# Kernel tuning notes

Hardware: AMD Instinct MI355X
Metric: run time of the kernel (lower is better)

The kernel has to match this reference:

```python
import jax, jax.numpy as jnp
import numpy as np

E = 256        # HP.EMBED_SIZE
R = 8          # number of derivation rules / MLPs
S = 512        # number of sequential derivation steps
N = 256        # nodes produced per step
N_INIT = 1024  # initial axiom (thax) embeddings
TOTAL = N_INIT + S * N  # 132096 rows in the vectors buffer
M = 65536      # masked nodes fed to eval_net


def setup_inputs() -> dict:
    key = jax.random.key(0)
    ks = jax.random.split(key, 12)
    rng = np.random.default_rng(0)

    init_vecs = jax.random.normal(ks[0], (N_INIT, E), jnp.float32)
    # rule MLPs: concat(2 parents) -> E (relu) -> E
    W1 = jax.random.normal(ks[1], (R, 2 * E, E), jnp.float32) * (1.0 / np.sqrt(2 * E))
    b1 = jnp.zeros((R, E), jnp.float32)
    W2 = jax.random.normal(ks[2], (R, E, E), jnp.float32) * (1.0 / np.sqrt(E))
    b2 = jnp.zeros((R, E), jnp.float32)
    # eval net: E -> E (relu) -> 1
    eval_W1 = jax.random.normal(ks[3], (E, E), jnp.float32) * (1.0 / np.sqrt(E))
    eval_b1 = jnp.zeros((E,), jnp.float32)
    eval_W2 = jax.random.normal(ks[4], (E, 1), jnp.float32) * (1.0 / np.sqrt(E))
    eval_b2 = jnp.zeros((1,), jnp.float32)

    # step s writes rows [N_INIT + s*N, N_INIT + (s+1)*N)
    ind_steps = (N_INIT + np.arange(S * N, dtype=np.int32)).reshape(S, N)
    # parents drawn causally from already-computed prefix [0, N_INIT + s*N)
    highs = (N_INIT + np.arange(S, dtype=np.int64) * N)[:, None, None]
    pars_ind_steps = (rng.random((S, N, 2)) * highs).astype(np.int32)
    rule_steps = rng.integers(0, R, size=(S,)).astype(np.int32)
    mask = rng.integers(0, TOTAL, size=(M,)).astype(np.int32)

    pos = jax.random.uniform(ks[5], (M,), jnp.float32)
    neg = jax.random.uniform(ks[6], (M,), jnp.float32)
    target = jnp.round(jax.random.uniform(ks[7], (M,), jnp.float32))

    return {
        'init_vecs': init_vecs, 'W1': W1, 'b1': b1, 'W2': W2, 'b2': b2,
        'eval_W1': eval_W1, 'eval_b1': eval_b1, 'eval_W2': eval_W2, 'eval_b2': eval_b2,
        'pos': pos, 'neg': neg, 'target': target,
        'ind_steps': jnp.asarray(ind_steps), 'pars_ind_steps': jnp.asarray(pars_ind_steps),
        'rule_steps': jnp.asarray(rule_steps), 'mask': jnp.asarray(mask),
    }


def reference(init_vecs, W1, b1, W2, b2, eval_W1, eval_b1, eval_W2, eval_b2,
              pos, neg, target, ind_steps, pars_ind_steps, rule_steps, mask):
    vectors = jnp.zeros((TOTAL, E), init_vecs.dtype).at[:N_INIT].set(init_vecs)

    def step(vec, xs):
        inds, pars, r = xs            # [N], [N,2], scalar rule id
        p = vec[pars].reshape(N, 2 * E)   # gather parents
        h = jax.nn.relu(p @ W1[r] + b1[r])
        out = h @ W2[r] + b2[r]
        return vec.at[inds].set(out), None  # scatter new node embeddings

    vectors, _ = jax.lax.scan(step, vectors, (ind_steps, pars_ind_steps, rule_steps))

    x = vectors[mask]
    val = (jax.nn.relu(x @ eval_W1 + eval_b1) @ eval_W2 + eval_b2)[:, 0]

    # pos_weight = POS_WEIGHT_EXTRA * tot_neg / tot_pos (constant w.r.t. grads)
    pw = jax.lax.stop_gradient(jnp.sum(neg) / jnp.maximum(jnp.sum(pos), 1.0))
    # BCEWithLogitsLoss(pos_weight, reduction='none')
    contrib = pw * target * jax.nn.softplus(-val) + (1.0 - target) * jax.nn.softplus(val)
    loss = jnp.sum((pos + neg) * contrib)
    posOK = jnp.sum(pos * (val >= 0))
    negOK = jnp.sum(neg * (val < 0))
    return loss, posOK, negOK
```

## Files before the change

kernel.cpp:

```cpp
#include <hip/hip_runtime.h>
#include <math.h>

#define EMB   256
#define TWOE  512
#define NINIT 1024
#define NSTEP 512
#define NPS   256
#define TOTAL (NINIT + NSTEP * NPS)
#define MM    65536
#define NNODE (NSTEP * NPS)
#define NKEY  2048
#define BTH   512
#define TROWS 32
#define CHK_SH  16384
#define RULE_SH (24 * CHK_SH)

typedef short s16x8 __attribute__((ext_vector_type(8)));
typedef float f32x4 __attribute__((ext_vector_type(4)));

#define OFF_VECH   0ull
#define OFF_VECL   ((size_t)TOTAL * EMB * 2)
#define OFF_VAL    (2ull * (size_t)TOTAL * EMB * 2)
#define OFF_CNT    (OFF_VAL + (size_t)MM * 4)
#define OFF_ACC    (OFF_CNT + 4096)
#define OFF_PW     (OFF_ACC + 64)
#define OFF_KCNT   (OFF_PW + 192)
#define OFF_KOFS   (OFF_KCNT + (size_t)NKEY * 4)
#define OFF_NL     (OFF_KOFS + (size_t)NKEY * 4)
#define OFF_BROWS  (OFF_NL + 256)
#define OFF_LVL8   (OFF_BROWS + (size_t)NNODE * 4)
#define OFF_WSPLIT (OFF_LVL8 + 132352)


__device__ __forceinline__ void store_dev_u32(unsigned* p, unsigned v) {
  asm volatile("global_store_dword %0, %1, off sc0 sc1" :: "v"(p), "v"(v) : "memory");
}
__device__ __forceinline__ void store_dev_b64(void* p, uint2 v) {
  asm volatile("global_store_dwordx2 %0, %1, off sc0 sc1" :: "v"(p), "v"(v) : "memory");
}
__device__ __forceinline__ void store_dev_b128(void* p, uint4 v) {
  store_dev_b64(p, make_uint2(v.x, v.y));
  store_dev_b64((char*)p + 8, make_uint2(v.z, v.w));
}
__device__ __forceinline__ unsigned load_dev_u32(const unsigned* p) {
  unsigned r;
  asm volatile("global_load_dword %0, %1, off sc0 sc1\n\ts_waitcnt vmcnt(0)"
               : "=v"(r) : "v"(p) : "memory");
  return r;
}

__device__ __forceinline__ void gbar_full(unsigned* gc, unsigned* gep) {
  asm volatile("s_waitcnt vmcnt(0)" ::: "memory");
  __syncthreads();
  if (threadIdx.x == 0) {
    unsigned old = __hip_atomic_fetch_add(gc, 1u, __ATOMIC_RELAXED, __HIP_MEMORY_SCOPE_AGENT);
    unsigned tgt = old / 256u + 1u;
    if ((old & 255u) == 255u) store_dev_u32(gep, tgt);
    else while (load_dev_u32(gep) < tgt) __builtin_amdgcn_s_sleep(1);
  }
  __syncthreads();
}

__device__ __forceinline__ void split8(const float* f, uint4& h4, uint4& l4) {
  unsigned hu[8], lu[8];
  #pragma unroll
  for (int i = 0; i < 8; ++i) {
    unsigned u = __builtin_bit_cast(unsigned, f[i]);
    float rh = __builtin_bit_cast(float, u & 0xffff0000u);
    float rl = f[i] - rh;
    hu[i] = u >> 16;
    lu[i] = __builtin_bit_cast(unsigned, rl) >> 16;
  }
  h4 = make_uint4(hu[0] | (hu[1] << 16), hu[2] | (hu[3] << 16),
                  hu[4] | (hu[5] << 16), hu[6] | (hu[7] << 16));
  l4 = make_uint4(lu[0] | (lu[1] << 16), lu[2] | (lu[3] << 16),
                  lu[4] | (lu[5] << 16), lu[6] | (lu[7] << 16));
}

__global__ void zero_scratch(unsigned* cnt, double* acc) {
  for (int i = threadIdx.x; i < 1024; i += 256) cnt[i] = 0u;
  if (threadIdx.x < 8) acc[threadIdx.x] = 0.0;
}

__global__ void init_convert(const float* __restrict__ src,
                             unsigned short* __restrict__ vh,
                             unsigned short* __restrict__ vl) {
  int slot = blockIdx.x * blockDim.x + threadIdx.x;
  float f[8];
  *(float4*)&f[0] = reinterpret_cast<const float4*>(src)[slot * 2];
  *(float4*)&f[4] = reinterpret_cast<const float4*>(src)[slot * 2 + 1];
  uint4 h4, l4;
  split8(f, h4, l4);
  *(uint4*)(vh + (size_t)slot * 8) = h4;
  *(uint4*)(vl + (size_t)slot * 8) = l4;
}

__global__ __launch_bounds__(512)
void presplit(const float* __restrict__ W1, const float* __restrict__ W2,
              short* __restrict__ Ws)
{
  const int blk = blockIdx.x;
  const int r = blk / 24, c = blk % 24;
  const float* src; int kbase;
  if (c < 16) { src = W1 + (size_t)r * TWOE * EMB; kbase = c * 32; }
  else        { src = W2 + (size_t)r * EMB * EMB;  kbase = (c - 16) * 32; }
  short* dst = Ws + (size_t)blk * CHK_SH;
  const int tid = threadIdx.x;
  #pragma unroll
  for (int u = 0; u < 2; ++u) {
    int qq = tid + u * 512;
    int g = qq >> 6, l = qq & 63;
    const float* p = src + (size_t)(kbase + ((l >> 4) << 3)) * EMB + (g << 4) + (l & 15);
    float f[8];
    #pragma unroll
    for (int i = 0; i < 8; ++i) f[i] = p[i * EMB];
    uint4 h4, l4;
    split8(f, h4, l4);
    *(uint4*)(dst + (size_t)qq * 8) = h4;
    *(uint4*)(dst + 8192 + (size_t)qq * 8) = l4;
  }
}

__global__ __launch_bounds__(256)
void prepass_levels(const int* __restrict__ pars, unsigned char* __restrict__ lvl8,
                    int* __restrict__ nlp)
{
  __shared__ unsigned char slvl[TOTAL];
  __shared__ int swmax[4];
  const int t = threadIdx.x;
  for (int i = t; i < NINIT; i += 256) slvl[i] = 0;
  __syncthreads();
  int Pa[8], Pb[8];
  #pragma unroll
  for (int w = 0; w < 8; ++w) {
    Pa[w] = pars[2 * (w * NPS + t)];
    Pb[w] = pars[2 * (w * NPS + t) + 1];
  }
  int lmax = 0;
  for (int s0 = 0; s0 < NSTEP; s0 += 8) {
    int Na[8], Nb[8];
    if (s0 + 8 < NSTEP) {
      #pragma unroll
      for (int w = 0; w < 8; ++w) {
        Na[w] = pars[2 * ((s0 + 8 + w) * NPS + t)];
        Nb[w] = pars[2 * ((s0 + 8 + w) * NPS + t) + 1];
      }
    } else {
      #pragma unroll
      for (int w = 0; w < 8; ++w) { Na[w] = 0; Nb[w] = 0; }
    }
    #pragma unroll
    for (int w = 0; w < 8; ++w) {
      int l1 = slvl[Pa[w]], l2 = slvl[Pb[w]];
      int lv = 1 + (l1 > l2 ? l1 : l2);
      slvl[NINIT + (s0 + w) * NPS + t] = (unsigned char)lv;
      if (lv > lmax) lmax = lv;
      __syncthreads();
    }
    #pragma unroll
    for (int w = 0; w < 8; ++w) { Pa[w] = Na[w]; Pb[w] = Nb[w]; }
  }
  const unsigned* sv = (const unsigned*)slvl;
  unsigned* gv = (unsigned*)lvl8;
  for (int i = t; i < TOTAL / 4; i += 256) gv[i] = sv[i];
  for (int o = 32; o; o >>= 1) lmax = max(lmax, __shfl_down(lmax, o));
  if ((t & 63) == 0) swmax[t >> 6] = lmax;
  __syncthreads();
  if (t == 0) {
    int m = 0;
    for (int w = 0; w < 4; ++w) m = max(m, swmax[w]);
    nlp[0] = m;
  }
}

__global__ __launch_bounds__(1024)
void prepass_bucket(const unsigned char* __restrict__ lvl8, const int* __restrict__ rules,
                    int* __restrict__ kcnt, int* __restrict__ kofs,
                    int* __restrict__ brows)
{
  __shared__ int scnt[NKEY];
  __shared__ int sofs[NKEY];
  const int t = threadIdx.x;
  for (int k = t; k < NKEY; k += 1024) scnt[k] = 0;
  __syncthreads();
  for (int i = t; i < NNODE; i += 1024) {
    int key = (int)lvl8[NINIT + i] * 8 + rules[i >> 8];
    atomicAdd(&scnt[key], 1);
  }
  __syncthreads();
  if (t == 0) {
    int run = 0;
    for (int k = 0; k < NKEY; ++k) {
      sofs[k] = run; kofs[k] = run; kcnt[k] = scnt[k]; run += scnt[k];
    }
  }
  __syncthreads();
  for (int i = t; i < NNODE; i += 1024) {
    int key = (int)lvl8[NINIT + i] * 8 + rules[i >> 8];
    int pos = atomicAdd(&sofs[key], 1);
    brows[pos] = i;
  }
}

__global__ __launch_bounds__(BTH, 1)
void scan_kernel(const short* __restrict__ Ws, const float* __restrict__ b1,
                 const float* __restrict__ b2, const int* __restrict__ pars,
                 unsigned short* __restrict__ vech, unsigned short* __restrict__ vecl,
                 const int* __restrict__ kcnt, const int* __restrict__ kofs,
                 const int* __restrict__ brows, const int* __restrict__ nlp,
                 unsigned* __restrict__ cnt)
{
  __shared__ float hL[TROWS][260];
  __shared__ int spar[2 * TROWS];
  __shared__ int sorow[TROWS];
  const int tid = threadIdx.x;
  const int bid = blockIdx.x;
  const int lane = tid & 63;
  const int w = tid >> 6;
  const int rw = w & 1, cwb = (w >> 1) << 2;
  const int row16 = lane & 15, kb8 = (lane >> 4) << 3;
  const int arow = (rw << 4) + row16;
  unsigned* gc  = cnt;
  unsigned* gep = cnt + 32;
  const int NL = nlp[0];
  const int xcd = bid & 7, jb = bid >> 3;

  for (int lv = 1; lv <= NL; ++lv) {
    int cum[9]; cum[0] = 0;
    int cnts[8], ofss[8];
    #pragma unroll
    for (int r = 0; r < 8; ++r) {
      int c = kcnt[lv * 8 + r];
      cnts[r] = c; ofss[r] = kofs[lv * 8 + r];
      cum[r + 1] = cum[r] + ((c + TROWS - 1) >> 5);
    }
    const int G = cum[8];
    const int q = G >> 3, rm = G & 7;
    const int Gx = q + (xcd < rm ? 1 : 0);
    const int sx = xcd * q + (xcd < rm ? xcd : rm);
    for (int j = jb; j < Gx; j += 32) {
      const int g = sx + j;
      int rr = 0;
      while (g >= cum[rr + 1]) ++rr;
      const int t0 = g - cum[rr];
      const int cnt_b = cnts[rr], ofs_b = ofss[rr];
      const int tbase = t0 * TROWS;
      const short* __restrict__ Wr = Ws + (size_t)rr * RULE_SH;

      __syncthreads();
      if (tid < 2 * TROWS) {
        int slot = tbase + (tid >> 1);
        if (slot >= cnt_b) slot = cnt_b - 1;
        int node = brows[ofs_b + slot];
        spar[tid] = pars[2 * node + (tid & 1)];
        if ((tid & 1) == 0) sorow[tid >> 1] = NINIT + node;
      }
      __syncthreads();
      const int par0 = spar[2 * arow], par1 = spar[2 * arow + 1];
      float b1v[4];
      #pragma unroll
      for (int g4 = 0; g4 < 4; ++g4)
        b1v[g4] = b1[rr * EMB + ((cwb + g4) << 4) + row16];

      uint4 ahA, alA;
      {
        size_t off = (size_t)par0 * EMB + kb8;
        ahA = *(const uint4*)(vech + off);
        alA = *(const uint4*)(vecl + off);
      }
      f32x4 acc[4] = {{0,0,0,0},{0,0,0,0},{0,0,0,0},{0,0,0,0}};
      #pragma unroll 2
      for (int c = 0; c < 16; ++c) {
        uint4 ahB = ahA, alB = alA;
        if (c < 15) {
          int kglob = (c + 1) * 32 + kb8;
          int par = (kglob >> 8) ? par1 : par0;
          size_t off = (size_t)par * EMB + (kglob & 255);
          ahB = *(const uint4*)(vech + off);
          alB = *(const uint4*)(vecl + off);
        }
        const short* ch = Wr + (size_t)c * CHK_SH;
        s16x8 Ah = __builtin_bit_cast(s16x8, ahA);
        s16x8 Al = __builtin_bit_cast(s16x8, alA);
        #pragma unroll
        for (int g4 = 0; g4 < 4; ++g4) {
          int gi = (cwb + g4) * 64 + lane;
          s16x8 Bh = *(const s16x8*)(ch + (size_t)gi * 8);
          s16x8 Bl = *(const s16x8*)(ch + 8192 + (size_t)gi * 8);
          acc[g4] = __builtin_amdgcn_mfma_f32_16x16x32_bf16(Ah, Bh, acc[g4], 0, 0, 0);
          acc[g4] = __builtin_amdgcn_mfma_f32_16x16x32_bf16(Ah, Bl, acc[g4], 0, 0, 0);
          acc[g4] = __builtin_amdgcn_mfma_f32_16x16x32_bf16(Al, Bh, acc[g4], 0, 0, 0);
        }
        ahA = ahB; alA = alB;
      }
      #pragma unroll
      for (int g4 = 0; g4 < 4; ++g4) {
        #pragma unroll
        for (int jj = 0; jj < 4; ++jj)
          hL[(rw << 4) + ((lane >> 4) << 2) + jj][((cwb + g4) << 4) + row16] =
              fmaxf(acc[g4][jj] + b1v[g4], 0.f);
      }
      __syncthreads();
      float b2v[4];
      #pragma unroll
      for (int g4 = 0; g4 < 4; ++g4)
        b2v[g4] = b2[rr * EMB + ((cwb + g4) << 4) + row16];
      f32x4 acc2[4] = {{0,0,0,0},{0,0,0,0},{0,0,0,0},{0,0,0,0}};
      for (int c2 = 0; c2 < 8; ++c2) {
        const short* ch = Wr + (size_t)(16 + c2) * CHK_SH;
        uint4 a2h, a2l;
        {
          float af[8];
          *(float4*)&af[0] = *(const float4*)&hL[arow][c2 * 32 + kb8];
          *(float4*)&af[4] = *(const float4*)&hL[arow][c2 * 32 + kb8 + 4];
          split8(af, a2h, a2l);
        }
        s16x8 Ah = __builtin_bit_cast(s16x8, a2h);
        s16x8 Al = __builtin_bit_cast(s16x8, a2l);
        #pragma unroll
        for (int g4 = 0; g4 < 4; ++g4) {
          int gi = (cwb + g4) * 64 + lane;
          s16x8 Bh = *(const s16x8*)(ch + (size_t)gi * 8);
          s16x8 Bl = *(const s16x8*)(ch + 8192 + (size_t)gi * 8);
          acc2[g4] = __builtin_amdgcn_mfma_f32_16x16x32_bf16(Ah, Bh, acc2[g4], 0, 0, 0);
          acc2[g4] = __builtin_amdgcn_mfma_f32_16x16x32_bf16(Ah, Bl, acc2[g4], 0, 0, 0);
          acc2[g4] = __builtin_amdgcn_mfma_f32_16x16x32_bf16(Al, Bh, acc2[g4], 0, 0, 0);
        }
      }
      __syncthreads();
      #pragma unroll
      for (int g4 = 0; g4 < 4; ++g4) {
        #pragma unroll
        for (int jj = 0; jj < 4; ++jj)
          hL[(rw << 4) + ((lane >> 4) << 2) + jj][((cwb + g4) << 4) + row16] =
              acc2[g4][jj] + b2v[g4];
      }
      __syncthreads();
      #pragma unroll
      for (int u = 0; u < 2; ++u) {
        int s = tid + u * 512;
        int row = s >> 5, c8 = (s & 31) * 8;
        float of[8];
        *(float4*)&of[0] = *(const float4*)&hL[row][c8];
        *(float4*)&of[4] = *(const float4*)&hL[row][c8 + 4];
        uint4 h4, l4;
        split8(of, h4, l4);
        if (tbase + row < cnt_b) {
          size_t off = (size_t)sorow[row] * EMB + c8;
          store_dev_b128(vech + off, h4);
          store_dev_b128(vecl + off, l4);
        }
      }
    }
    gbar_full(gc, gep);
  }
}

__global__ void reduce_pn(const float* __restrict__ pos, const float* __restrict__ neg,
                          double* acc) {
  double sp = 0.0, sn = 0.0;
  for (int m = blockIdx.x * blockDim.x + threadIdx.x; m < MM; m += gridDim.x * blockDim.x) {
    sp += (double)pos[m]; sn += (double)neg[m];
  }
  for (int o = 32; o; o >>= 1) { sp += __shfl_down(sp, o); sn += __shfl_down(sn, o); }
  __shared__ double rp[4], rn[4];
  int wid = threadIdx.x >> 6, lane = threadIdx.x & 63;
  if (lane == 0) { rp[wid] = sp; rn[wid] = sn; }
  __syncthreads();
  if (threadIdx.x == 0) {
    double tp = 0.0, tn = 0.0;
    for (int w = 0; w < 4; ++w) { tp += rp[w]; tn += rn[w]; }
    atomicAdd(&acc[0], tp); atomicAdd(&acc[1], tn);
  }
}

__global__ void pw_kernel(const double* __restrict__ acc, float* __restrict__ pw) {
  pw[0] = (float)(acc[1] / fmax(acc[0], 1.0));
}

__global__ __launch_bounds__(256)
void eval_kernel(const unsigned short* __restrict__ vh, const unsigned short* __restrict__ vl,
                 const int* __restrict__ mask,
                 const float* __restrict__ eW1, const float* __restrict__ eb1,
                 const float* __restrict__ eW2, const float* __restrict__ eb2,
                 float* __restrict__ val)
{
  __shared__ float xL[64][36];
  __shared__ float wLx[32][260];
  __shared__ int mrow[64];
  const int tid = threadIdx.x;
  const int a = tid >> 4, b = tid & 15;
  const int m0 = blockIdx.x * 64;
  if (tid < 64) mrow[tid] = mask[m0 + tid];
  __syncthreads();

  float acc[4][16];
  #pragma unroll
  for (int i = 0; i < 4; ++i)
    #pragma unroll
    for (int j = 0; j < 16; ++j) acc[i][j] = 0.f;

  for (int c = 0; c < 8; ++c) {
    const int e0 = c * 32;
    for (int idx = tid; idx < 64 * 4; idx += 256) {
      int rr = idx >> 2, u = idx & 3;
      size_t off = (size_t)mrow[rr] * EMB + e0 + u * 8;
      uint4 hv = *(const uint4*)(vh + off);
      uint4 lv = *(const uint4*)(vl + off);
      const unsigned* hu = (const unsigned*)&hv;
      const unsigned* lu = (const unsigned*)&lv;
      float fo[8];
      #pragma unroll
      for (int jj = 0; jj < 4; ++jj) {
        fo[2 * jj] = __builtin_bit_cast(float, (hu[jj] & 0xffffu) << 16) +
                     __builtin_bit_cast(float, (lu[jj] & 0xffffu) << 16);
        fo[2 * jj + 1] = __builtin_bit_cast(float, hu[jj] & 0xffff0000u) +
                         __builtin_bit_cast(float, lu[jj] & 0xffff0000u);
      }
      *(float4*)&xL[rr][u * 8] = *(float4*)&fo[0];
      *(float4*)&xL[rr][u * 8 + 4] = *(float4*)&fo[4];
    }
    for (int idx = tid; idx < 32 * 64; idx += 256) {
      int e = idx >> 6, k4 = idx & 63;
      reinterpret_cast<float4*>(&wLx[e][0])[k4] =
          reinterpret_cast<const float4*>(eW1 + (size_t)(e0 + e) * EMB)[k4];
    }
    __syncthreads();
    #pragma unroll 4
    for (int e = 0; e < 32; ++e) {
      float xs[4];
      #pragma unroll
      for (int rr = 0; rr < 4; ++rr) xs[rr] = xL[a * 4 + rr][e];
      const float4* wr = reinterpret_cast<const float4*>(&wLx[e][0]) + b * 4;
      float wk[16];
      *reinterpret_cast<float4*>(&wk[0])  = wr[0];
      *reinterpret_cast<float4*>(&wk[4])  = wr[1];
      *reinterpret_cast<float4*>(&wk[8])  = wr[2];
      *reinterpret_cast<float4*>(&wk[12]) = wr[3];
      #pragma unroll
      for (int rr = 0; rr < 4; ++rr)
        #pragma unroll
        for (int kk = 0; kk < 16; ++kk)
          acc[rr][kk] = fmaf(xs[rr], wk[kk], acc[rr][kk]);
    }
    __syncthreads();
  }

  float eb2v = eb2[0];
  float pv[4];
  #pragma unroll
  for (int rr = 0; rr < 4; ++rr) {
    float s = 0.f;
    #pragma unroll
    for (int kk = 0; kk < 16; ++kk) {
      float h = acc[rr][kk] + eb1[b * 16 + kk];
      h = fmaxf(h, 0.f);
      s += h * eW2[b * 16 + kk];
    }
    pv[rr] = s;
  }
  #pragma unroll
  for (int m = 1; m < 16; m <<= 1) {
    #pragma unroll
    for (int rr = 0; rr < 4; ++rr) pv[rr] += __shfl_xor(pv[rr], m);
  }
  if (b == 0) {
    #pragma unroll
    for (int rr = 0; rr < 4; ++rr) val[m0 + a * 4 + rr] = pv[rr] + eb2v;
  }
}

__global__ void loss_kernel(const float* __restrict__ val, const float* __restrict__ pos,
                            const float* __restrict__ neg, const float* __restrict__ tgt,
                            const float* __restrict__ pwp, double* acc)
{
  const float pw = pwp[0];
  double l = 0.0, pk = 0.0, nk = 0.0;
  for (int m = blockIdx.x * blockDim.x + threadIdx.x; m < MM; m += gridDim.x * blockDim.x) {
    float v = val[m], p = pos[m], n = neg[m], t = tgt[m];
    float lp = log1pf(expf(-fabsf(v)));
    float spn = fmaxf(-v, 0.f) + lp;
    float spp = fmaxf(v, 0.f) + lp;
    float contrib = pw * t * spn + (1.f - t) * spp;
    l += (double)((p + n) * contrib);
    if (v >= 0.f) pk += (double)p; else nk += (double)n;
  }
  for (int o = 32; o; o >>= 1) {
    l += __shfl_down(l, o); pk += __shfl_down(pk, o); nk += __shfl_down(nk, o);
  }
  __shared__ double s0[4], s1[4], s2[4];
  int wid = threadIdx.x >> 6, lane = threadIdx.x & 63;
  if (lane == 0) { s0[wid] = l; s1[wid] = pk; s2[wid] = nk; }
  __syncthreads();
  if (threadIdx.x == 0) {
    double ta = 0.0, tb = 0.0, tc = 0.0;
    for (int w = 0; w < 4; ++w) { ta += s0[w]; tb += s1[w]; tc += s2[w]; }
    atomicAdd(&acc[2], ta); atomicAdd(&acc[3], tb); atomicAdd(&acc[4], tc);
  }
}

__global__ void writeout(const double* __restrict__ acc, float* __restrict__ out) {
  if (threadIdx.x == 0) {
    out[0] = (float)acc[2];
    out[1] = (float)acc[3];
    out[2] = (float)acc[4];
  }
}

extern "C" void kernel_launch(void* const* d_in, const int* in_sizes, int n_in,
                              void* d_out, int out_size, void* d_ws, size_t ws_size,
                              hipStream_t stream)
{
  (void)in_sizes; (void)n_in; (void)out_size; (void)ws_size;
  const float* init_vecs = (const float*)d_in[0];
  const float* W1  = (const float*)d_in[1];
  const float* b1  = (const float*)d_in[2];
  const float* W2  = (const float*)d_in[3];
  const float* b2  = (const float*)d_in[4];
  const float* eW1 = (const float*)d_in[5];
  const float* eb1 = (const float*)d_in[6];
  const float* eW2 = (const float*)d_in[7];
  const float* eb2 = (const float*)d_in[8];
  const float* pos = (const float*)d_in[9];
  const float* neg = (const float*)d_in[10];
  const float* tgt = (const float*)d_in[11];
  const int* pars  = (const int*)d_in[13];
  const int* rules = (const int*)d_in[14];
  const int* mask  = (const int*)d_in[15];

  char* ws = (char*)d_ws;
  unsigned short* vech = (unsigned short*)(ws + OFF_VECH);
  unsigned short* vecl = (unsigned short*)(ws + OFF_VECL);
  float*    val   = (float*)(ws + OFF_VAL);
  unsigned* cnt   = (unsigned*)(ws + OFF_CNT);
  double*   acc   = (double*)(ws + OFF_ACC);
  float*    pw    = (float*)(ws + OFF_PW);
  int*      kcnt  = (int*)(ws + OFF_KCNT);
  int*      kofs  = (int*)(ws + OFF_KOFS);
  int*      nlp   = (int*)(ws + OFF_NL);
  int*      brows = (int*)(ws + OFF_BROWS);
  unsigned char* lvl8 = (unsigned char*)(ws + OFF_LVL8);
  short*    Ws    = (short*)(ws + OFF_WSPLIT);

  zero_scratch<<<1, 256, 0, stream>>>(cnt, acc);
  prepass_levels<<<1, 256, 0, stream>>>(pars, lvl8, nlp);
  prepass_bucket<<<1, 1024, 0, stream>>>(lvl8, rules, kcnt, kofs, brows);
  init_convert<<<128, 256, 0, stream>>>(init_vecs, vech, vecl);
  presplit<<<192, 512, 0, stream>>>(W1, W2, Ws);
  scan_kernel<<<256, BTH, 0, stream>>>(Ws, b1, b2, pars, vech, vecl,
                                       kcnt, kofs, brows, nlp, cnt);
  reduce_pn<<<128, 256, 0, stream>>>(pos, neg, acc);
  pw_kernel<<<1, 1, 0, stream>>>(acc, pw);
  eval_kernel<<<1024, 256, 0, stream>>>(vech, vecl, mask, eW1, eb1, eW2, eb2, val);
  loss_kernel<<<128, 256, 0, stream>>>(val, pos, neg, tgt, pw, acc);
  writeout<<<1, 1, 0, stream>>>(acc, (float*)d_out);
}
```

Measured before the change: 1.323 ms.

## Replace grid barrier with per-level tile counters and LDS double-buffer weights

The global barrier after each dependency level is replaced by per-level completion counters, so blocks wait only until the previous level's tiles are finished. Weight chunks are staged through a double-buffered LDS pipeline instead of being read straight from global memory in the MFMA loops. Hidden activations are kept in LDS as split bf16 hi/lo rather than fp32, and the level and bucket prepasses are merged into one kernel. The pw kernel is folded into the loss kernel. LDS use grows to about 100KB, and there are extra syncthreads per chunk.

```diff
diff --git a/kernel.cpp b/kernel.cpp
--- a/kernel.cpp
+++ b/kernel.cpp
@@ -23,13 +23,12 @@
 #define OFF_VAL    (2ull * (size_t)TOTAL * EMB * 2)
 #define OFF_CNT    (OFF_VAL + (size_t)MM * 4)
 #define OFF_ACC    (OFF_CNT + 4096)
-#define OFF_PW     (OFF_ACC + 64)
-#define OFF_KCNT   (OFF_PW + 192)
+#define OFF_KCNT   (OFF_ACC + 256)
 #define OFF_KOFS   (OFF_KCNT + (size_t)NKEY * 4)
 #define OFF_NL     (OFF_KOFS + (size_t)NKEY * 4)
-#define OFF_BROWS  (OFF_NL + 256)
-#define OFF_LVL8   (OFF_BROWS + (size_t)NNODE * 4)
-#define OFF_WSPLIT (OFF_LVL8 + 132352)
+#define OFF_TPL    (OFF_NL + 256)
+#define OFF_BROWS  (OFF_TPL + 4096)
+#define OFF_WSPLIT (OFF_BROWS + (size_t)NNODE * 4)
 
 
 __device__ __forceinline__ void store_dev_u32(unsigned* p, unsigned v) {
@@ -47,18 +46,6 @@
   asm volatile("global_load_dword %0, %1, off sc0 sc1\n\ts_waitcnt vmcnt(0)"
                : "=v"(r) : "v"(p) : "memory");
   return r;
-}
-
-__device__ __forceinline__ void gbar_full(unsigned* gc, unsigned* gep) {
-  asm volatile("s_waitcnt vmcnt(0)" ::: "memory");
-  __syncthreads();
-  if (threadIdx.x == 0) {
-    unsigned old = __hip_atomic_fetch_add(gc, 1u, __ATOMIC_RELAXED, __HIP_MEMORY_SCOPE_AGENT);
-    unsigned tgt = old / 256u + 1u;
-    if ((old & 255u) == 255u) store_dev_u32(gep, tgt);
-    else while (load_dev_u32(gep) < tgt) __builtin_amdgcn_s_sleep(1);
-  }
-  __syncthreads();
 }
 
 __device__ __forceinline__ void split8(const float* f, uint4& h4, uint4& l4) {
@@ -76,9 +63,16 @@
   l4 = make_uint4(lu[0] | (lu[1] << 16), lu[2] | (lu[3] << 16),
                   lu[4] | (lu[5] << 16), lu[6] | (lu[7] << 16));
 }
-
-__global__ void zero_scratch(unsigned* cnt, double* acc) {
-  for (int i = threadIdx.x; i < 1024; i += 256) cnt[i] = 0u;
+__device__ __forceinline__ void split1(float f, short& hi, short& lo) {
+  unsigned u = __builtin_bit_cast(unsigned, f);
+  float rh = __builtin_bit_cast(float, u & 0xffff0000u);
+  float rl = f - rh;
+  hi = (short)(u >> 16);
+  lo = (short)(__builtin_bit_cast(unsigned, rl) >> 16);
+}
+
+__global__ void zero_scratch(unsigned* done, double* acc) {
+  if (threadIdx.x < 256) done[threadIdx.x] = 0u;
   if (threadIdx.x < 8) acc[threadIdx.x] = 0.0;
 }
 
@@ -121,70 +115,62 @@
   }
 }
 
-__global__ __launch_bounds__(256)
-void prepass_levels(const int* __restrict__ pars, unsigned char* __restrict__ lvl8,
-                    int* __restrict__ nlp)
+__global__ __launch_bounds__(1024)
+void prepass(const int* __restrict__ pars, const int* __restrict__ rules,
+             int* __restrict__ kcnt, int* __restrict__ kofs,
+             int* __restrict__ brows, int* __restrict__ tpl, int* __restrict__ nlp)
 {
   __shared__ unsigned char slvl[TOTAL];
-  __shared__ int swmax[4];
+  __shared__ int scnt[NKEY];
+  __shared__ int sofs[NKEY];
+  __shared__ int swmax[16];
   const int t = threadIdx.x;
-  for (int i = t; i < NINIT; i += 256) slvl[i] = 0;
+  for (int i = t; i < NINIT; i += 1024) slvl[i] = 0;
+  for (int k = t; k < NKEY; k += 1024) scnt[k] = 0;
   __syncthreads();
   int Pa[8], Pb[8];
-  #pragma unroll
-  for (int w = 0; w < 8; ++w) {
-    Pa[w] = pars[2 * (w * NPS + t)];
-    Pb[w] = pars[2 * (w * NPS + t) + 1];
+  if (t < NPS) {
+    #pragma unroll
+    for (int w = 0; w < 8; ++w) {
+      Pa[w] = pars[2 * (w * NPS + t)];
+      Pb[w] = pars[2 * (w * NPS + t) + 1];
+    }
   }
   int lmax = 0;
   for (int s0 = 0; s0 < NSTEP; s0 += 8) {
     int Na[8], Nb[8];
-    if (s0 + 8 < NSTEP) {
+    if (t < NPS && s0 + 8 < NSTEP) {
       #pragma unroll
       for (int w = 0; w < 8; ++w) {
         Na[w] = pars[2 * ((s0 + 8 + w) * NPS + t)];
         Nb[w] = pars[2 * ((s0 + 8 + w) * NPS + t) + 1];
       }
-    } else {
-      #pragma unroll
-      for (int w = 0; w < 8; ++w) { Na[w] = 0; Nb[w] = 0; }
     }
     #pragma unroll
     for (int w = 0; w < 8; ++w) {
-      int l1 = slvl[Pa[w]], l2 = slvl[Pb[w]];
-      int lv = 1 + (l1 > l2 ? l1 : l2);
-      slvl[NINIT + (s0 + w) * NPS + t] = (unsigned char)lv;
-      if (lv > lmax) lmax = lv;
-      __syncthreads();
-    }
-    #pragma unroll
-    for (int w = 0; w < 8; ++w) { Pa[w] = Na[w]; Pb[w] = Nb[w]; }
-  }
-  const unsigned* sv = (const unsigned*)slvl;
-  unsigned* gv = (unsigned*)lvl8;
-  for (int i = t; i < TOTAL / 4; i += 256) gv[i] = sv[i];
+      if (t < NPS) {
+        int l1 = slvl[Pa[w]], l2 = slvl[Pb[w]];
+        int lv = 1 + (l1 > l2 ? l1 : l2);
+        slvl[NINIT + (s0 + w) * NPS + t] = (unsigned char)lv;
+        if (lv > lmax) lmax = lv;
+      }
+      __syncthreads();
+    }
+    if (t < NPS && s0 + 8 < NSTEP) {
+      #pragma unroll
+      for (int w = 0; w < 8; ++w) { Pa[w] = Na[w]; Pb[w] = Nb[w]; }
+    }
+  }
   for (int o = 32; o; o >>= 1) lmax = max(lmax, __shfl_down(lmax, o));
   if ((t & 63) == 0) swmax[t >> 6] = lmax;
   __syncthreads();
   if (t == 0) {
     int m = 0;
-    for (int w = 0; w < 4; ++w) m = max(m, swmax[w]);
+    for (int w = 0; w < 16; ++w) m = max(m, swmax[w]);
     nlp[0] = m;
   }
-}
-
-__global__ __launch_bounds__(1024)
-void prepass_bucket(const unsigned char* __restrict__ lvl8, const int* __restrict__ rules,
-                    int* __restrict__ kcnt, int* __restrict__ kofs,
-                    int* __restrict__ brows)
-{
-  __shared__ int scnt[NKEY];
-  __shared__ int sofs[NKEY];
-  const int t = threadIdx.x;
-  for (int k = t; k < NKEY; k += 1024) scnt[k] = 0;
-  __syncthreads();
   for (int i = t; i < NNODE; i += 1024) {
-    int key = (int)lvl8[NINIT + i] * 8 + rules[i >> 8];
+    int key = (int)slvl[NINIT + i] * 8 + rules[i >> 8];
     atomicAdd(&scnt[key], 1);
   }
   __syncthreads();
@@ -195,8 +181,14 @@
     }
   }
   __syncthreads();
+  if (t < 256) {
+    int s = 0;
+    #pragma unroll
+    for (int r = 0; r < 8; ++r) s += (scnt[t * 8 + r] + TROWS - 1) >> 5;
+    tpl[t] = s;
+  }
   for (int i = t; i < NNODE; i += 1024) {
-    int key = (int)lvl8[NINIT + i] * 8 + rules[i >> 8];
+    int key = (int)slvl[NINIT + i] * 8 + rules[i >> 8];
     int pos = atomicAdd(&sofs[key], 1);
     brows[pos] = i;
   }
@@ -207,10 +199,12 @@
                  const float* __restrict__ b2, const int* __restrict__ pars,
                  unsigned short* __restrict__ vech, unsigned short* __restrict__ vecl,
                  const int* __restrict__ kcnt, const int* __restrict__ kofs,
-                 const int* __restrict__ brows, const int* __restrict__ nlp,
-                 unsigned* __restrict__ cnt)
+                 const int* __restrict__ brows, const int* __restrict__ tpl,
+                 const int* __restrict__ nlp, unsigned* __restrict__ done)
 {
-  __shared__ float hL[TROWS][260];
+  __shared__ short wB[2][CHK_SH];
+  __shared__ short hH[TROWS][264];
+  __shared__ short hLo[TROWS][264];
   __shared__ int spar[2 * TROWS];
   __shared__ int sorow[TROWS];
   const int tid = threadIdx.x;
@@ -220,12 +214,17 @@
   const int rw = w & 1, cwb = (w >> 1) << 2;
   const int row16 = lane & 15, kb8 = (lane >> 4) << 3;
   const int arow = (rw << 4) + row16;
-  unsigned* gc  = cnt;
-  unsigned* gep = cnt + 32;
+  const int hrow = (rw << 4) + ((lane >> 4) << 2);
   const int NL = nlp[0];
   const int xcd = bid & 7, jb = bid >> 3;
 
   for (int lv = 1; lv <= NL; ++lv) {
+    if (tid == 0 && lv > 1) {
+      const unsigned need = (unsigned)tpl[lv - 1];
+      const unsigned* dp = done + (lv - 1);
+      while (load_dev_u32(dp) < need) __builtin_amdgcn_s_sleep(2);
+    }
+    __syncthreads();
     int cum[9]; cum[0] = 0;
     int cnts[8], ofss[8];
     #pragma unroll
@@ -255,104 +254,147 @@
         spar[tid] = pars[2 * node + (tid & 1)];
         if ((tid & 1) == 0) sorow[tid >> 1] = NINIT + node;
       }
+      uint4 st0, st1, st2, st3;
+      {
+        const short* cs = Wr;
+        st0 = *(const uint4*)(cs + (size_t)tid * 8);
+        st1 = *(const uint4*)(cs + (size_t)(512 + tid) * 8);
+        st2 = *(const uint4*)(cs + 8192 + (size_t)tid * 8);
+        st3 = *(const uint4*)(cs + 8192 + (size_t)(512 + tid) * 8);
+      }
       __syncthreads();
       const int par0 = spar[2 * arow], par1 = spar[2 * arow + 1];
-      float b1v[4];
-      #pragma unroll
-      for (int g4 = 0; g4 < 4; ++g4)
+      float b1v[4], b2v[4];
+      #pragma unroll
+      for (int g4 = 0; g4 < 4; ++g4) {
         b1v[g4] = b1[rr * EMB + ((cwb + g4) << 4) + row16];
-
+        b2v[g4] = b2[rr * EMB + ((cwb + g4) << 4) + row16];
+      }
       uint4 ahA, alA;
       {
         size_t off = (size_t)par0 * EMB + kb8;
         ahA = *(const uint4*)(vech + off);
         alA = *(const uint4*)(vecl + off);
       }
+      {
+        *(uint4*)&wB[0][tid * 8] = st0;
+        *(uint4*)&wB[0][(512 + tid) * 8] = st1;
+        *(uint4*)&wB[0][8192 + tid * 8] = st2;
+        *(uint4*)&wB[0][8192 + (512 + tid) * 8] = st3;
+      }
+      __syncthreads();
       f32x4 acc[4] = {{0,0,0,0},{0,0,0,0},{0,0,0,0},{0,0,0,0}};
-      #pragma unroll 2
+      int curb = 0;
       for (int c = 0; c < 16; ++c) {
+        {
+          const short* cs = Wr + (size_t)(c + 1) * CHK_SH;
+          st0 = *(const uint4*)(cs + (size_t)tid * 8);
+          st1 = *(const uint4*)(cs + (size_t)(512 + tid) * 8);
+          st2 = *(const uint4*)(cs + 8192 + (size_t)tid * 8);
+          st3 = *(const uint4*)(cs + 8192 + (size_t)(512 + tid) * 8);
+        }
         uint4 ahB = ahA, alB = alA;
         if (c < 15) {
-          int kglob = (c + 1) * 32 + kb8;
-          int par = (kglob >> 8) ? par1 : par0;
-          size_t off = (size_t)par * EMB + (kglob & 255);
+          int kg = (c + 1) * 32 + kb8;
+          int par = (kg >> 8) ? par1 : par0;
+          size_t off = (size_t)par * EMB + (kg & 255);
           ahB = *(const uint4*)(vech + off);
           alB = *(const uint4*)(vecl + off);
         }
-        const short* ch = Wr + (size_t)c * CHK_SH;
-        s16x8 Ah = __builtin_bit_cast(s16x8, ahA);
-        s16x8 Al = __builtin_bit_cast(s16x8, alA);
+        {
+          s16x8 Ah = __builtin_bit_cast(s16x8, ahA);
+          s16x8 Al = __builtin_bit_cast(s16x8, alA);
+          #pragma unroll
+          for (int g4 = 0; g4 < 4; ++g4) {
+            int gi = (cwb + g4) * 64 + lane;
+            s16x8 Bh = *(const s16x8*)&wB[curb][gi * 8];
+            s16x8 Bl = *(const s16x8*)&wB[curb][8192 + gi * 8];
+            acc[g4] = __builtin_amdgcn_mfma_f32_16x16x32_bf16(Ah, Bh, acc[g4], 0, 0, 0);
+            acc[g4] = __builtin_amdgcn_mfma_f32_16x16x32_bf16(Ah, Bl, acc[g4], 0, 0, 0);
+            acc[g4] = __builtin_amdgcn_mfma_f32_16x16x32_bf16(Al, Bh, acc[g4], 0, 0, 0);
+          }
+        }
+        if (c == 15) {
+          #pragma unroll
+          for (int g4 = 0; g4 < 4; ++g4) {
+            #pragma unroll
+            for (int jj = 0; jj < 4; ++jj) {
+              int col = ((cwb + g4) << 4) + row16;
+              short hi, lo;
+              split1(fmaxf(acc[g4][jj] + b1v[g4], 0.f), hi, lo);
+              hH[hrow + jj][col] = hi; hLo[hrow + jj][col] = lo;
+            }
+          }
+        }
+        {
+          *(uint4*)&wB[curb ^ 1][tid * 8] = st0;
+          *(uint4*)&wB[curb ^ 1][(512 + tid) * 8] = st1;
+          *(uint4*)&wB[curb ^ 1][8192 + tid * 8] = st2;
+          *(uint4*)&wB[curb ^ 1][8192 + (512 + tid) * 8] = st3;
+        }
+        __syncthreads();
+        curb ^= 1;
+        ahA = ahB; alA = alB;
+      }
+      f32x4 acc2[4] = {{0,0,0,0},{0,0,0,0},{0,0,0,0},{0,0,0,0}};
+      for (int c2 = 0; c2 < 8; ++c2) {
+        if (c2 < 7) {
+          const short* cs = Wr + (size_t)(17 + c2) * CHK_SH;
+          st0 = *(const uint4*)(cs + (size_t)tid * 8);
+          st1 = *(const uint4*)(cs + (size_t)(512 + tid) * 8);
+          st2 = *(const uint4*)(cs + 8192 + (size_t)tid * 8);
+          st3 = *(const uint4*)(cs + 8192 + (size_t)(512 + tid) * 8);
+        }
+        const int kc = c2 * 32 + kb8;
+        s16x8 Ah = *(const s16x8*)&hH[arow][kc];
+        s16x8 Al = *(const s16x8*)&hLo[arow][kc];
         #pragma unroll
         for (int g4 = 0; g4 < 4; ++g4) {
           int gi = (cwb + g4) * 64 + lane;
-          s16x8 Bh = *(const s16x8*)(ch + (size_t)gi * 8);
-          s16x8 Bl = *(const s16x8*)(ch + 8192 + (size_t)gi * 8);
-          acc[g4] = __builtin_amdgcn_mfma_f32_16x16x32_bf16(Ah, Bh, acc[g4], 0, 0, 0);
-          acc[g4] = __builtin_amdgcn_mfma_f32_16x16x32_bf16(Ah, Bl, acc[g4], 0, 0, 0);
-          acc[g4] = __builtin_amdgcn_mfma_f32_16x16x32_bf16(Al, Bh, acc[g4], 0, 0, 0);
-        }
-        ahA = ahB; alA = alB;
-      }
-      #pragma unroll
-      for (int g4 = 0; g4 < 4; ++g4) {
-        #pragma unroll
-        for (int jj = 0; jj < 4; ++jj)
-          hL[(rw << 4) + ((lane >> 4) << 2) + jj][((cwb + g4) << 4) + row16] =
-              fmaxf(acc[g4][jj] + b1v[g4], 0.f);
-      }
-      __syncthreads();
-      float b2v[4];
-      #pragma unroll
-      for (int g4 = 0; g4 < 4; ++g4)
-        b2v[g4] = b2[rr * EMB + ((cwb + g4) << 4) + row16];
-      f32x4 acc2[4] = {{0,0,0,0},{0,0,0,0},{0,0,0,0},{0,0,0,0}};
-      for (int c2 = 0; c2 < 8; ++c2) {
-        const short* ch = Wr + (size_t)(16 + c2) * CHK_SH;
-        uint4 a2h, a2l;
-        {
-          float af[8];
-          *(float4*)&af[0] = *(const float4*)&hL[arow][c2 * 32 + kb8];
-          *(float4*)&af[4] = *(const float4*)&hL[arow][c2 * 32 + kb8 + 4];
-          split8(af, a2h, a2l);
-        }
-        s16x8 Ah = __builtin_bit_cast(s16x8, a2h);
-        s16x8 Al = __builtin_bit_cast(s16x8, a2l);
-        #pragma unroll
-        for (int g4 = 0; g4 < 4; ++g4) {
-          int gi = (cwb + g4) * 64 + lane;
-          s16x8 Bh = *(const s16x8*)(ch + (size_t)gi * 8);
-          s16x8 Bl = *(const s16x8*)(ch + 8192 + (size_t)gi * 8);
+          s16x8 Bh = *(const s16x8*)&wB[curb][gi * 8];
+          s16x8 Bl = *(const s16x8*)&wB[curb][8192 + gi * 8];
           acc2[g4] = __builtin_amdgcn_mfma_f32_16x16x32_bf16(Ah, Bh, acc2[g4], 0, 0, 0);
           acc2[g4] = __builtin_amdgcn_mfma_f32_16x16x32_bf16(Ah, Bl, acc2[g4], 0, 0, 0);
           acc2[g4] = __builtin_amdgcn_mfma_f32_16x16x32_bf16(Al, Bh, acc2[g4], 0, 0, 0);
         }
+        if (c2 < 7) {
+          *(uint4*)&wB[curb ^ 1][tid * 8] = st0;
+          *(uint4*)&wB[curb ^ 1][(512 + tid) * 8] = st1;
+          *(uint4*)&wB[curb ^ 1][8192 + tid * 8] = st2;
+          *(uint4*)&wB[curb ^ 1][8192 + (512 + tid) * 8] = st3;
+          __syncthreads();
+          curb ^= 1;
+        }
       }
       __syncthreads();
       #pragma unroll
       for (int g4 = 0; g4 < 4; ++g4) {
         #pragma unroll
-        for (int jj = 0; jj < 4; ++jj)
-          hL[(rw << 4) + ((lane >> 4) << 2) + jj][((cwb + g4) << 4) + row16] =
-              acc2[g4][jj] + b2v[g4];
+        for (int jj = 0; jj < 4; ++jj) {
+          int col = ((cwb + g4) << 4) + row16;
+          short hi, lo;
+          split1(acc2[g4][jj] + b2v[g4], hi, lo);
+          hH[hrow + jj][col] = hi; hLo[hrow + jj][col] = lo;
+        }
       }
       __syncthreads();
       #pragma unroll
       for (int u = 0; u < 2; ++u) {
         int s = tid + u * 512;
         int row = s >> 5, c8 = (s & 31) * 8;
-        float of[8];
-        *(float4*)&of[0] = *(const float4*)&hL[row][c8];
-        *(float4*)&of[4] = *(const float4*)&hL[row][c8 + 4];
-        uint4 h4, l4;
-        split8(of, h4, l4);
+        uint4 h4 = *(const uint4*)&hH[row][c8];
+        uint4 l4 = *(const uint4*)&hLo[row][c8];
         if (tbase + row < cnt_b) {
           size_t off = (size_t)sorow[row] * EMB + c8;
           store_dev_b128(vech + off, h4);
           store_dev_b128(vecl + off, l4);
         }
       }
-    }
-    gbar_full(gc, gep);
+      asm volatile("s_waitcnt vmcnt(0)" ::: "memory");
+      __syncthreads();
+      if (tid == 0)
+        __hip_atomic_fetch_add(done + lv, 1u, __ATOMIC_RELAXED, __HIP_MEMORY_SCOPE_AGENT);
+    }
   }
 }
 
@@ -372,10 +414,6 @@
     for (int w = 0; w < 4; ++w) { tp += rp[w]; tn += rn[w]; }
     atomicAdd(&acc[0], tp); atomicAdd(&acc[1], tn);
   }
-}
-
-__global__ void pw_kernel(const double* __restrict__ acc, float* __restrict__ pw) {
-  pw[0] = (float)(acc[1] / fmax(acc[0], 1.0));
 }
 
 __global__ __launch_bounds__(256)
@@ -472,9 +510,9 @@
 
 __global__ void loss_kernel(const float* __restrict__ val, const float* __restrict__ pos,
                             const float* __restrict__ neg, const float* __restrict__ tgt,
-                            const float* __restrict__ pwp, double* acc)
+                            double* acc)
 {
-  const float pw = pwp[0];
+  const float pw = (float)(acc[1] / fmax(acc[0], 1.0));
   double l = 0.0, pk = 0.0, nk = 0.0;
   for (int m = blockIdx.x * blockDim.x + threadIdx.x; m < MM; m += gridDim.x * blockDim.x) {
     float v = val[m], p = pos[m], n = neg[m], t = tgt[m];
@@ -532,26 +570,23 @@
   unsigned short* vech = (unsigned short*)(ws + OFF_VECH);
   unsigned short* vecl = (unsigned short*)(ws + OFF_VECL);
   float*    val   = (float*)(ws + OFF_VAL);
-  unsigned* cnt   = (unsigned*)(ws + OFF_CNT);
+  unsigned* done  = (unsigned*)(ws + OFF_CNT);
   double*   acc   = (double*)(ws + OFF_ACC);
-  float*    pw    = (float*)(ws + OFF_PW);
   int*      kcnt  = (int*)(ws + OFF_KCNT);
   int*      kofs  = (int*)(ws + OFF_KOFS);
   int*      nlp   = (int*)(ws + OFF_NL);
+  int*      tpl   = (int*)(ws + OFF_TPL);
   int*      brows = (int*)(ws + OFF_BROWS);
-  unsigned char* lvl8 = (unsigned char*)(ws + OFF_LVL8);
   short*    Ws    = (short*)(ws + OFF_WSPLIT);
 
-  zero_scratch<<<1, 256, 0, stream>>>(cnt, acc);
-  prepass_levels<<<1, 256, 0, stream>>>(pars, lvl8, nlp);
-  prepass_bucket<<<1, 1024, 0, stream>>>(lvl8, rules, kcnt, kofs, brows);
+  zero_scratch<<<1, 256, 0, stream>>>(done, acc);
+  prepass<<<1, 1024, 0, stream>>>(pars, rules, kcnt, kofs, brows, tpl, nlp);
   init_convert<<<128, 256, 0, stream>>>(init_vecs, vech, vecl);
   presplit<<<192, 512, 0, stream>>>(W1, W2, Ws);
   scan_kernel<<<256, BTH, 0, stream>>>(Ws, b1, b2, pars, vech, vecl,
-                                       kcnt, kofs, brows, nlp, cnt);
+                                       kcnt, kofs, brows, tpl, nlp, done);
   reduce_pn<<<128, 256, 0, stream>>>(pos, neg, acc);
-  pw_kernel<<<1, 1, 0, stream>>>(acc, pw);
   eval_kernel<<<1024, 256, 0, stream>>>(vech, vecl, mask, eW1, eb1, eW2, eb2, val);
-  loss_kernel<<<128, 256, 0, stream>>>(val, pos, neg, tgt, pw, acc);
+  loss_kernel<<<128, 256, 0, stream>>>(val, pos, neg, tgt, acc);
   writeout<<<1, 1, 0, stream>>>(acc, (float*)d_out);
 }
```

After: 1.221 ms. -7.7%, faster.
